# Kernel tuning notes

Hardware: AMD Instinct MI355X
Metric: run time of the kernel (lower is better)

Reference implementation:

```python
import jax, jax.numpy as jnp
import numpy as np

# Static config (matches init_kwargs)
B, L, D = 4, 4096, 1024
K, H, M = 32, 32, 1           # key heads, per-head dim, num_thetas
A = 4                          # num_anchor_heads
CK = 4                         # conv_kernel_size (causal depthwise)
D_INNER = D                    # expand_factor = 1
ZC = 2 * D_INNER + K           # in_proj output channels = 2080
FLAT = K * H * M
SPLIT = H * M


def setup_inputs() -> dict:
    key = jax.random.key(0)
    ks = jax.random.split(key, 6)
    x = jax.random.normal(ks[0], (B, L, D), jnp.float32)
    # in_proj Dense(d_inner*2 + K, no bias): [D, ZC]
    W_in = jax.random.normal(ks[1], (D, ZC), jnp.float32) / np.sqrt(D)
    # depthwise causal conv kernel, flax 'WIO' layout: [CK, 1, ZC]
    conv_kernel = jax.random.normal(ks[2], (CK, 1, ZC), jnp.float32) / np.sqrt(CK)
    # theta init for M == 1: linspace grid with alternating signs
    grid = np.linspace(0.1, 1.5, K * H).reshape(1, 1, K, H, 1)
    signs = np.resize([1.0, -1.0], grid.shape)
    theta = jnp.asarray(grid * signs, jnp.float32)
    # inverse-softplus of geomspace slopes
    decay_slopes = jnp.asarray(np.log(np.exp(np.geomspace(0.001, 0.1, K - A)) - 1.0), jnp.float32)
    anchor_slopes = jnp.asarray(np.log(np.exp(np.geomspace(0.01, 0.1, A)) - 1.0), jnp.float32)
    score_scale = jnp.ones((K,), jnp.float32)
    lim = float(np.sqrt(6.0 / (SPLIT + H)))  # glorot uniform
    W_re = jax.random.uniform(ks[3], (SPLIT, H), jnp.float32, -lim, lim)
    W_im = jax.random.uniform(ks[4], (SPLIT, H), jnp.float32, -lim, lim)
    norm_scale = jnp.ones((2 * SPLIT,), jnp.float32)
    W_out = jax.random.normal(ks[5], (D_INNER, D), jnp.float32) / np.sqrt(D_INNER)
    return {"x": x, "W_in": W_in, "conv_kernel": conv_kernel, "theta": theta,
            "decay_slopes": decay_slopes, "anchor_slopes": anchor_slopes,
            "score_scale": score_scale, "W_re": W_re, "W_im": W_im,
            "norm_scale": norm_scale, "W_out": W_out}


def reference(x, W_in, conv_kernel, theta, decay_slopes, anchor_slopes,
              score_scale, W_re, W_im, norm_scale, W_out):
    b, l, _ = x.shape
    z = x @ W_in                                           # [b,l,ZC]
    # causal depthwise conv (padding (CK-1, 0), groups == channels)
    z = jax.lax.conv_general_dilated(
        z, conv_kernel, window_strides=(1,), padding=((CK - 1, 0),),
        dimension_numbers=('NWC', 'WIO', 'NWC'), feature_group_count=ZC)
    x_val = z[..., :D_INNER].reshape(b, l, K, H)
    x_gate = jax.nn.silu(z[..., D_INNER:2 * D_INNER])      # [b,l,d_inner]
    s_raw = z[..., -K:].reshape(b, l, K, 1)
    # ALiBi-style log time weights: decay heads look back, anchor heads decay from start
    pos = jnp.arange(l, dtype=jnp.float32)
    dist = jnp.maximum(jnp.float32(l - 1) - pos, 0.0)      # maxlen=None -> l
    log_w = jnp.concatenate([
        -jax.nn.softplus(decay_slopes).reshape(1, 1, -1, 1) * dist[None, :, None, None],
        -jax.nn.softplus(anchor_slopes).reshape(1, 1, -1, 1) * pos[None, :, None, None],
    ], axis=2)                                             # [1,l,K,1]
    p_w = jnp.exp(score_scale[None, None, :, None] * s_raw + log_w)  # [b,l,K,1]
    # complex phase features
    phi = x_val[..., None] * theta                         # [b,l,K,H,M]
    pwb = p_w[..., None]
    num_re_in = (pwb * jnp.cos(phi)).reshape(b, l, FLAT)
    num_im_in = (pwb * jnp.sin(phi)).reshape(b, l, FLAT)
    merged = jnp.concatenate([p_w.squeeze(-1), num_re_in, num_im_in], axis=-1)
    cs = jnp.cumsum(merged, axis=1)                        # causal prefix sum over seq
    den, num_re, num_im = jnp.split(cs, [K, K + FLAT], axis=-1)
    inv_den = 1.0 / jnp.maximum(den.reshape(b, l, K, 1), 1e-4)
    re = num_re.reshape(b, l, K, SPLIT) * inv_den
    im = num_im.reshape(b, l, K, SPLIT) * inv_den
    # running RMS normalization over complex features
    mean_sq = (jnp.sum(re * re, -1) + jnp.sum(im * im, -1)) / (2 * SPLIT)
    rs = jax.lax.rsqrt(mean_sq[..., None] + 1e-5)
    y = (re * rs * norm_scale[:SPLIT]) @ W_re + (im * rs * norm_scale[SPLIT:]) @ W_im  # [b,l,K,H]
    return (y.reshape(b, l, D_INNER) * x_gate) @ W_out
```

## Files before the change

kernel.cpp:

```cpp
#include <hip/hip_runtime.h>
#include <hip/hip_bf16.h>
#include <math.h>

#define BB 4
#define LL 4096
#define DD 1024
#define KK 32
#define HH 32
#define AA 4
#define CKK 4
#define DI 1024
#define ZC 2080
#define FLATC 1024
#define BL (BB * LL)
#define ZLD 2080
#define NPAD 2176

#define CCH 32
#define NCHK (LL / CCH)

#define GLD 1136
#define KLD 1080

typedef unsigned short u16;
typedef __attribute__((ext_vector_type(8))) short s16x8;
typedef __attribute__((ext_vector_type(4))) float f32x4;

__device__ __forceinline__ u16 f2bf(float f) {
  union { float f; unsigned int u; } v; v.f = f;
  unsigned int r = (v.u + 0x7FFFu + ((v.u >> 16) & 1u)) >> 16;
  return (u16)r;
}
__device__ __forceinline__ float bf2f(u16 u) {
  union { unsigned int i; float f; } x; x.i = ((unsigned int)u) << 16; return x.f;
}
__device__ __forceinline__ void gl_lds16(const void* g, void* l) {
  __builtin_amdgcn_global_load_lds(
      (const __attribute__((address_space(1))) unsigned int*)g,
      (__attribute__((address_space(3))) unsigned int*)l, 16, 0, 0);
}

__global__ __launch_bounds__(256) void cast_bf16_kernel(
    const float* __restrict__ src, u16* __restrict__ dst, int n) {
  const int i = (blockIdx.x * 256 + threadIdx.x) * 8;
  if (i >= n) return;
  float4 a = *(const float4*)(src + i);
  float4 b = *(const float4*)(src + i + 4);
  s16x8 v;
  v[0] = (short)f2bf(a.x); v[1] = (short)f2bf(a.y);
  v[2] = (short)f2bf(a.z); v[3] = (short)f2bf(a.w);
  v[4] = (short)f2bf(b.x); v[5] = (short)f2bf(b.y);
  v[6] = (short)f2bf(b.z); v[7] = (short)f2bf(b.w);
  *(s16x8*)(dst + i) = v;
}

__global__ __launch_bounds__(256) void transpose_cast_kernel(
    const float* __restrict__ src, u16* __restrict__ dst,
    int R, int C, int Cpad) {
  __shared__ float t[32][33];
  const int tid = threadIdx.x;
  const int r0 = blockIdx.x * 32, c0 = blockIdx.y * 32;
  const int lr = tid >> 5, lc = tid & 31;
#pragma unroll
  for (int i = 0; i < 4; ++i) {
    const int r = r0 + i * 8 + lr, c = c0 + lc;
    float v = 0.f;
    if (r < R && c < C) v = src[(size_t)r * C + c];
    t[lc][i * 8 + lr] = v;
  }
  __syncthreads();
#pragma unroll
  for (int i = 0; i < 4; ++i) {
    const int dr = c0 + i * 8 + lr;
    const int dc = r0 + lc;
    if (dr < Cpad && dc < R) dst[(size_t)dr * R + dc] = f2bf(t[i * 8 + lr][lc]);
  }
}

#define FENCE() asm volatile("" ::: "memory")
#define SBAR() do { FENCE(); __builtin_amdgcn_s_barrier(); FENCE(); } while (0)
#define VMCNT6() asm volatile("s_waitcnt vmcnt(6)" ::: "memory")

#define RA(s, h) (((s) * 2 + (h)) * 8192)
#define RB(s, h) (32768 + ((s) * 2 + (h)) * 8192)

template <int OUT_BF16>
__global__ __launch_bounds__(512, 2) void gemm256_8ph(
    const u16* __restrict__ A, const u16* __restrict__ Bt, void* __restrict__ C,
    int lda, int ldb, int ldc, int Kd, int Ncols) {
  __shared__ u16 lds[65536];
  const int tid = threadIdx.x;
  const int lane = tid & 63, wv = tid >> 6;
  const int wm = wv >> 2, wn = wv & 3;
  const int lm = lane & 15, lq = lane >> 4;
  const int bm = blockIdx.x * 256, bn = blockIdx.y * 256;
  const int NT = Kd >> 6;
  const int NT2 = NT >> 1;

  const int rofs = wv * 8 + (lane >> 3);
  const int cel = ((lane & 7) ^ (lane >> 3)) * 8;

  auto stageH = [&](const u16* __restrict__ G, int rowBase, int ld, int kt,
                    int regU16) {
    const u16* g0 = G + (size_t)(rowBase + rofs) * ld + (kt << 6) + cel;
    gl_lds16(g0, &lds[regU16 + wv * 512]);
    const u16* g1 = G + (size_t)(rowBase + 64 + rofs) * ld + (kt << 6) + cel;
    gl_lds16(g1, &lds[regU16 + 4096 + wv * 512]);
  };

  s16x8 Af[4][2], Bf[4][2];
  f32x4 acc[8][4];
  const f32x4 z4 = {0.f, 0.f, 0.f, 0.f};
#pragma unroll
  for (int i = 0; i < 8; ++i)
#pragma unroll
    for (int j = 0; j < 4; ++j) acc[i][j] = z4;

  const int xorw = (lm & 7) << 3;

#define DSA(s, mh)                                                          \
  _Pragma("unroll") for (int f = 0; f < 4; ++f)                             \
  _Pragma("unroll") for (int ks = 0; ks < 2; ++ks)                          \
    Af[f][ks] = *(const s16x8*)&lds[RA(s, wm) +                             \
      (((((mh) * 4 + f) * 16 + lm) * 64 + ((ks * 32 + lq * 8) ^ xorw)))];

#define DSB(s)                                                              \
  _Pragma("unroll") for (int f = 0; f < 4; ++f)                             \
  _Pragma("unroll") for (int ks = 0; ks < 2; ++ks)                          \
    Bf[f][ks] = *(const s16x8*)&lds[RB(s, wn >> 1) +                        \
      ((((wn & 1) * 64 + f * 16 + lm) * 64 + ((ks * 32 + lq * 8) ^ xorw)))];

#define QUAD(mh, nh)                                                        \
  do {                                                                      \
    __builtin_amdgcn_s_setprio(1);                                          \
    _Pragma("unroll") for (int f = 0; f < 4; ++f)                           \
    _Pragma("unroll") for (int n = 0; n < 2; ++n)                           \
    _Pragma("unroll") for (int ks = 0; ks < 2; ++ks)                        \
      acc[(mh) * 4 + f][(nh) * 2 + n] =                                     \
          __builtin_amdgcn_mfma_f32_16x16x32_bf16(                          \
              Af[f][ks], Bf[(nh) * 2 + n][ks],                              \
              acc[(mh) * 4 + f][(nh) * 2 + n], 0, 0, 0);                    \
    __builtin_amdgcn_s_setprio(0);                                          \
  } while (0)

  stageH(A, bm, lda, 0, RA(0, 0));
  stageH(A, bm + 128, lda, 0, RA(0, 1));
  stageH(Bt, bn, ldb, 0, RB(0, 0));
  stageH(Bt, bn + 128, ldb, 0, RB(0, 1));
  stageH(Bt, bn, ldb, 1, RB(1, 0));
  stageH(Bt, bn + 128, ldb, 1, RB(1, 1));
  stageH(A, bm, lda, 1, RA(1, 0));
  VMCNT6();
  SBAR();

#pragma unroll 1
  for (int t = 0; t < NT2; ++t) {
    const int T2 = 2 * t + 2, T3 = 2 * t + 3;
    DSA(0, 0); DSB(0);
    stageH(A, bm + 128, lda, 2 * t + 1, RA(1, 1));
    SBAR();
    QUAD(0, 0);
    SBAR();
    if (T2 < NT) stageH(Bt, bn, ldb, T2, RB(0, 0));
    SBAR();
    QUAD(0, 1);
    SBAR();
    DSA(0, 1);
    if (T2 < NT) stageH(Bt, bn + 128, ldb, T2, RB(0, 1));
    SBAR();
    QUAD(1, 0);
    SBAR();
    if (T2 < NT) stageH(A, bm, lda, T2, RA(0, 0));
    SBAR();
    QUAD(1, 1);
    VMCNT6();
    SBAR();
    DSA(1, 0); DSB(1);
    if (T2 < NT) stageH(A, bm + 128, lda, T2, RA(0, 1));
    SBAR();
    QUAD(0, 0);
    SBAR();
    if (T3 < NT) stageH(Bt, bn, ldb, T3, RB(1, 0));
    SBAR();
    QUAD(0, 1);
    SBAR();
    DSA(1, 1);
    if (T3 < NT) stageH(Bt, bn + 128, ldb, T3, RB(1, 1));
    SBAR();
    QUAD(1, 0);
    SBAR();
    if (T3 < NT) stageH(A, bm, lda, T3, RA(1, 0));
    SBAR();
    QUAD(1, 1);
    VMCNT6();
    SBAR();
  }

#pragma unroll
  for (int f = 0; f < 8; ++f) {
#pragma unroll
    for (int n = 0; n < 4; ++n) {
#pragma unroll
      for (int r = 0; r < 4; ++r) {
        const int row = bm + wm * 128 + f * 16 + lq * 4 + r;
        const int col = bn + wn * 64 + n * 16 + lm;
        if (col < Ncols) {
          if (OUT_BF16)
            ((u16*)C)[(size_t)row * ldc + col] = f2bf(acc[f][n][r]);
          else
            ((float*)C)[(size_t)row * ldc + col] = acc[f][n][r];
        }
      }
    }
  }
#undef DSA
#undef DSB
#undef QUAD
}

__global__ __launch_bounds__(256) void score_gemm(
    const u16* __restrict__ A, const u16* __restrict__ Bt,
    u16* __restrict__ z) {
  __shared__ u16 As[8192];
  __shared__ u16 Bs[2048];
  const int tid = threadIdx.x;
  const int lane = tid & 63, wv = tid >> 6;
  const int lm = lane & 15, lq = lane >> 4;
  const int bm = blockIdx.x * 128;

  const f32x4 z4 = {0.f, 0.f, 0.f, 0.f};
  f32x4 acc[2][2];
#pragma unroll
  for (int i = 0; i < 2; ++i)
#pragma unroll
    for (int j = 0; j < 2; ++j) acc[i][j] = z4;

  for (int k0 = 0; k0 < DD; k0 += 64) {
    __syncthreads();
#pragma unroll
    for (int t = 0; t < 5; ++t) {
      const int idx = wv * 5 + t;
      if (idx < 16) {
        const int mt = idx >> 1, kt = idx & 1;
        const u16* g = A + (size_t)(bm + mt * 16 + lm) * DD + k0 + kt * 32 + lq * 8;
        gl_lds16(g, &As[idx * 512]);
      } else {
        const int bidx = idx - 16;
        const int nt = bidx >> 1, kt = bidx & 1;
        const u16* g = Bt + (size_t)(2048 + nt * 16 + lm) * DD + k0 + kt * 32 + lq * 8;
        gl_lds16(g, &Bs[bidx * 512]);
      }
    }
    __syncthreads();
#pragma unroll
    for (int kt = 0; kt < 2; ++kt) {
      s16x8 af[2], bfb[2];
#pragma unroll
      for (int i = 0; i < 2; ++i) {
        const int mt = wv * 2 + i;
        af[i] = *(const s16x8*)&As[(mt * 2 + kt) * 512 + lane * 8];
        bfb[i] = *(const s16x8*)&Bs[(i * 2 + kt) * 512 + lane * 8];
      }
#pragma unroll
      for (int i = 0; i < 2; ++i)
#pragma unroll
        for (int j = 0; j < 2; ++j)
          acc[i][j] = __builtin_amdgcn_mfma_f32_16x16x32_bf16(af[i], bfb[j], acc[i][j], 0, 0, 0);
    }
  }
#pragma unroll
  for (int i = 0; i < 2; ++i)
#pragma unroll
    for (int j = 0; j < 2; ++j)
#pragma unroll
      for (int r = 0; r < 4; ++r) {
        const int row = bm + wv * 32 + i * 16 + lq * 4 + r;
        const int col = 2048 + j * 16 + lm;
        z[(size_t)row * ZLD + col] = f2bf(acc[i][j][r]);
      }
}

__global__ __launch_bounds__(256) void conv_feat_scan(
    const u16* __restrict__ z, const float* __restrict__ kern,
    const float* __restrict__ theta, const float* __restrict__ decay,
    const float* __restrict__ anchor, const float* __restrict__ sscale,
    float* __restrict__ merged, float* __restrict__ part) {
  __shared__ float pbuf[CCH][KK];
  const int tid = threadIdx.x;
  const int r0 = blockIdx.x * CCH;
  const bool first = ((r0 & (LL - 1)) == 0);
  const int chunk = blockIdx.x;

#pragma unroll
  for (int q = 0; q < 4; ++q) {
    const int item = q * 256 + tid;
    const int row = item >> 5, k = item & 31;
    float v = 0.f;
#pragma unroll
    for (int w = 0; w < CKK; ++w) {
      const int g = row + w;
      float zv = 0.f;
      if (!(first && g < 3))
        zv = bf2f(z[(size_t)(r0 - 3 + g) * ZLD + 2048 + k]);
      v = fmaf(zv, kern[w * ZC + 2048 + k], v);
    }
    const int l = (r0 + row) & (LL - 1);
    const float slope = (k < KK - AA) ? decay[k] : anchor[k - (KK - AA)];
    const float sp = log1pf(__expf(slope));
    const float lw = (k < KK - AA) ? (-sp * (float)(LL - 1 - l)) : (-sp * (float)l);
    pbuf[row][k] = __expf(sscale[k] * v + lw);
  }
  __syncthreads();

  if (tid < KK) {
    float run = 0.f;
#pragma unroll
    for (int row = 0; row < CCH; ++row) {
      run += pbuf[row][tid];
      merged[(size_t)(r0 + row) * ZC + tid] = run;
    }
    part[(size_t)chunk * ZC + tid] = run;
  }

#pragma unroll 1
  for (int it = 0; it < 4; ++it) {
    const int c = it * 256 + tid;
    const float kw0 = kern[0 * ZC + c], kw1 = kern[1 * ZC + c];
    const float kw2 = kern[2 * ZC + c], kw3 = kern[3 * ZC + c];
    const float th = theta[c];
    const int head = c >> 5;
    float h0 = 0.f, h1 = 0.f, h2 = 0.f;
    if (!first) {
      h0 = bf2f(z[(size_t)(r0 - 3) * ZLD + c]);
      h1 = bf2f(z[(size_t)(r0 - 2) * ZLD + c]);
      h2 = bf2f(z[(size_t)(r0 - 1) * ZLD + c]);
    }
    float sre = 0.f, sim = 0.f;
#pragma unroll 4
    for (int row = 0; row < CCH; ++row) {
      const float h3 = bf2f(z[(size_t)(r0 + row) * ZLD + c]);
      float v = h0 * kw0;
      v = fmaf(h1, kw1, v);
      v = fmaf(h2, kw2, v);
      v = fmaf(h3, kw3, v);
      h0 = h1; h1 = h2; h2 = h3;
      const float phi = v * th;
      float sv, cv;
      __sincosf(phi, &sv, &cv);
      const float p = pbuf[row][head];
      sre = fmaf(p, cv, sre);
      sim = fmaf(p, sv, sim);
      float* mrow = merged + (size_t)(r0 + row) * ZC;
      mrow[KK + c] = sre;
      mrow[KK + FLATC + c] = sim;
    }
    part[(size_t)chunk * ZC + KK + c] = sre;
    part[(size_t)chunk * ZC + KK + FLATC + c] = sim;
  }
}

__global__ __launch_bounds__(256) void scan_offsets_kernel(float* __restrict__ part) {
  const int c = blockIdx.x * 256 + threadIdx.x;
  const int b = blockIdx.z;
  if (c >= ZC) return;
  float run = 0.f;
#pragma unroll 8
  for (int i = 0; i < NCHK; ++i) {
    const size_t idx = ((size_t)b * NCHK + i) * ZC + c;
    const float t = part[idx];
    part[idx] = run;
    run += t;
  }
}

__global__ __launch_bounds__(256) void wprime_kernel(
    const float* __restrict__ W_re, const float* __restrict__ W_im,
    const float* __restrict__ ns, u16* __restrict__ wp) {
  const int i = blockIdx.x * 256 + threadIdx.x;
  if (i < 1024) wp[i] = f2bf(ns[i >> 5] * W_re[i]);
  else {
    const int j = i - 1024;
    wp[i] = f2bf(ns[32 + (j >> 5)] * W_im[j]);
  }
}

__global__ __launch_bounds__(256) void norm_head_mfma(
    float* merged, const u16* __restrict__ z, const float* __restrict__ kern,
    const u16* __restrict__ wp, const float* __restrict__ part) {
  __shared__ u16 zw[11 * GLD];
  __shared__ float skern[4 * KLD];
  const int tid = threadIdx.x;
  const int r0 = blockIdx.x * 8;
  const bool first = ((r0 & (LL - 1)) == 0);
  const int lane = tid & 63, wv = tid >> 6;
  const int lm = lane & 15, lq = lane >> 4;
  const float* po = part + (size_t)(blockIdx.x >> 2) * ZC;

  for (int idx = tid; idx < 11 * 128; idx += 256) {
    const int i = idx >> 7, c8 = idx & 127;
    s16x8 v = {0, 0, 0, 0, 0, 0, 0, 0};
    if (!(first && i < 3))
      v = *(const s16x8*)(z + (size_t)(r0 - 3 + i) * ZLD + 1024 + c8 * 8);
    *(s16x8*)&zw[i * GLD + c8 * 8 + (c8 >> 4) * 16] = v;
  }
  for (int idx = tid; idx < 4 * 256; idx += 256) {
    const int w = idx >> 8, c4 = idx & 255;
    float4 v = *(const float4*)(kern + w * ZC + 1024 + c4 * 4);
    *(float4*)&skern[w * KLD + c4 * 4 + (c4 >> 5) * 8] = v;
  }

  s16x8 bre[2], bim[2];
#pragma unroll
  for (int nt = 0; nt < 2; ++nt)
#pragma unroll
    for (int jj = 0; jj < 8; ++jj) {
      bre[nt][jj] = (short)wp[(lq * 8 + jj) * 32 + nt * 16 + lm];
      bim[nt][jj] = (short)wp[1024 + (lq * 8 + jj) * 32 + nt * 16 + lm];
    }
  __syncthreads();

  const f32x4 z4 = {0.f, 0.f, 0.f, 0.f};
#pragma unroll 1
  for (int rr2 = 0; rr2 < 2; ++rr2) {
    const int rr = wv * 2 + rr2;
    const int bl = r0 + rr;
    float* row = merged + (size_t)bl * ZC;
    const float den0 = row[lm] + po[lm];
    const float den1 = row[16 + lm] + po[16 + lm];

#pragma unroll
    for (int khalf = 0; khalf < 2; ++khalf) {
      const int co = KK + (khalf * 16 + lm) * 32 + lq * 8;
      const float* rp = row + co;
      const float* pp = po + co;
      float4 ra = *(const float4*)rp;
      float4 rb = *(const float4*)(rp + 4);
      float4 ia = *(const float4*)(rp + FLATC);
      float4 ib = *(const float4*)(rp + FLATC + 4);
      float4 qa = *(const float4*)pp;
      float4 qb = *(const float4*)(pp + 4);
      float4 ja = *(const float4*)(pp + FLATC);
      float4 jb = *(const float4*)(pp + FLATC + 4);
      ra.x += qa.x; ra.y += qa.y; ra.z += qa.z; ra.w += qa.w;
      rb.x += qb.x; rb.y += qb.y; rb.z += qb.z; rb.w += qb.w;
      ia.x += ja.x; ia.y += ja.y; ia.z += ja.z; ia.w += ja.w;
      ib.x += jb.x; ib.y += jb.y; ib.z += jb.z; ib.w += jb.w;

      float ssq = ra.x * ra.x + ra.y * ra.y + ra.z * ra.z + ra.w * ra.w +
                  rb.x * rb.x + rb.y * rb.y + rb.z * rb.z + rb.w * rb.w +
                  ia.x * ia.x + ia.y * ia.y + ia.z * ia.z + ia.w * ia.w +
                  ib.x * ib.x + ib.y * ib.y + ib.z * ib.z + ib.w * ib.w;
      ssq += __shfl_xor(ssq, 16);
      ssq += __shfl_xor(ssq, 32);
      const float den = khalf ? den1 : den0;
      const float inv = 1.0f / fmaxf(den, 1e-4f);
      const float scale = inv * rsqrtf(ssq * inv * inv * (1.0f / 64.0f) + 1e-5f);

      s16x8 afr, afi;
      afr[0] = (short)f2bf(ra.x * scale); afr[1] = (short)f2bf(ra.y * scale);
      afr[2] = (short)f2bf(ra.z * scale); afr[3] = (short)f2bf(ra.w * scale);
      afr[4] = (short)f2bf(rb.x * scale); afr[5] = (short)f2bf(rb.y * scale);
      afr[6] = (short)f2bf(rb.z * scale); afr[7] = (short)f2bf(rb.w * scale);
      afi[0] = (short)f2bf(ia.x * scale); afi[1] = (short)f2bf(ia.y * scale);
      afi[2] = (short)f2bf(ia.z * scale); afi[3] = (short)f2bf(ia.w * scale);
      afi[4] = (short)f2bf(ib.x * scale); afi[5] = (short)f2bf(ib.y * scale);
      afi[6] = (short)f2bf(ib.z * scale); afi[7] = (short)f2bf(ib.w * scale);

      f32x4 acc[2];
#pragma unroll
      for (int nt = 0; nt < 2; ++nt) {
        acc[nt] = __builtin_amdgcn_mfma_f32_16x16x32_bf16(afr, bre[nt], z4, 0, 0, 0);
        acc[nt] = __builtin_amdgcn_mfma_f32_16x16x32_bf16(afi, bim[nt], acc[nt], 0, 0, 0);
      }

      u16* grow = (u16*)row;
#pragma unroll
      for (int nt = 0; nt < 2; ++nt) {
#pragma unroll
        for (int r = 0; r < 4; ++r) {
          const int k = khalf * 16 + lq * 4 + r;
          const int o = k * 32 + nt * 16 + lm;
          const int sk = o + (o >> 7) * 8;
          const int sz = o + (o >> 7) * 16;
          float gv = bf2f(zw[(rr + 0) * GLD + sz]) * skern[0 * KLD + sk];
          gv = fmaf(bf2f(zw[(rr + 1) * GLD + sz]), skern[1 * KLD + sk], gv);
          gv = fmaf(bf2f(zw[(rr + 2) * GLD + sz]), skern[2 * KLD + sk], gv);
          gv = fmaf(bf2f(zw[(rr + 3) * GLD + sz]), skern[3 * KLD + sk], gv);
          const float sil = gv * (1.0f / (1.0f + __expf(-gv)));
          grow[o] = f2bf(acc[nt][r] * sil);
        }
      }
    }
  }
}

extern "C" void kernel_launch(void* const* d_in, const int* in_sizes, int n_in,
                              void* d_out, int out_size, void* d_ws, size_t ws_size,
                              hipStream_t stream) {
  const float* x      = (const float*)d_in[0];
  const float* W_in   = (const float*)d_in[1];
  const float* kern   = (const float*)d_in[2];
  const float* theta  = (const float*)d_in[3];
  const float* decay  = (const float*)d_in[4];
  const float* anchor = (const float*)d_in[5];
  const float* sscale = (const float*)d_in[6];
  const float* W_re   = (const float*)d_in[7];
  const float* W_im   = (const float*)d_in[8];
  const float* nscale = (const float*)d_in[9];
  const float* W_out  = (const float*)d_in[10];
  float* out = (float*)d_out;

  char* w = (char*)d_ws;
  float* merged = (float*)w;
  u16* xbf = (u16*)w;
  u16* zbf = (u16*)(w + (size_t)BL * ZC * 4);
  u16* wobt = zbf;
  u16* wp = (u16*)(w + (size_t)BL * ZC * 4 + (size_t)BL * ZLD * 2);
  u16* wbt = wp + 2048;
  float* part = (float*)wbt;

  cast_bf16_kernel<<<dim3(BL * DD / 8 / 256), 256, 0, stream>>>(x, xbf, BL * DD);
  transpose_cast_kernel<<<dim3(32, 68), 256, 0, stream>>>(W_in, wbt, DD, ZC, NPAD);
  wprime_kernel<<<dim3(8), 256, 0, stream>>>(W_re, W_im, nscale, wp);

  score_gemm<<<dim3(BL / 128), 256, 0, stream>>>(xbf, wbt, zbf);

  gemm256_8ph<1><<<dim3(BL / 256, 8), 512, 0, stream>>>(
      xbf, wbt, zbf, DD, DD, ZLD, DD, ZC);

  conv_feat_scan<<<dim3(BL / CCH), 256, 0, stream>>>(
      zbf, kern, theta, decay, anchor, sscale, merged, part);

  {
    dim3 grid2((ZC + 255) / 256, 1, BB);
    scan_offsets_kernel<<<grid2, 256, 0, stream>>>(part);
  }

  norm_head_mfma<<<dim3(BL / 8), 256, 0, stream>>>(merged, zbf, kern, wp, part);

  transpose_cast_kernel<<<dim3(32, 32), 256, 0, stream>>>(W_out, wobt, DI, DD, DD);
  gemm256_8ph<0><<<dim3(BL / 256, DD / 256), 512, 0, stream>>>(
      (const u16*)merged, wobt, out, 2 * ZC, DI, DD, DI, DD);
}
```

Before: 364.2 us.

## Fuse conv, features, scan and norm-head per head with two-pass segmented scan

Replaces the materialized fp32 prefix-sum buffer (merged), the chunk-offset scan and the separate norm/head kernel with a head-major two-pass design. The in_proj GEMM and score GEMM now write z in a [b,k,l,h] layout. A first pass computes per-segment totals of the weighted cos/sin features and densities. A small scan turns those totals into segment offsets. A second pass recomputes the conv and phase features, scans them in shared memory, normalizes, applies W_re/W_im in registers, gates with the SiLU conv output, and writes bf16 directly. This removes the large fp32 intermediate write/read traffic. The cost is computing the sincos features twice, only 512 blocks each walking 1024 rows sequentially, and scattered stores in the GEMM epilogue.

```diff
diff --git a/kernel.cpp b/kernel.cpp
--- a/kernel.cpp
+++ b/kernel.cpp
@@ -13,14 +13,9 @@
 #define ZC 2080
 #define FLATC 1024
 #define BL (BB * LL)
-#define ZLD 2080
 #define NPAD 2176
-
-#define CCH 32
-#define NCHK (LL / CCH)
-
-#define GLD 1136
-#define KLD 1080
+#define SEG 4
+#define FST 68
 
 typedef unsigned short u16;
 typedef __attribute__((ext_vector_type(8))) short s16x8;
@@ -84,10 +79,10 @@
 #define RA(s, h) (((s) * 2 + (h)) * 8192)
 #define RB(s, h) (32768 + ((s) * 2 + (h)) * 8192)
 
-template <int OUT_BF16>
+template <int MODE>
 __global__ __launch_bounds__(512, 2) void gemm256_8ph(
     const u16* __restrict__ A, const u16* __restrict__ Bt, void* __restrict__ C,
-    int lda, int ldb, int ldc, int Kd, int Ncols) {
+    void* __restrict__ C2, int lda, int ldb, int ldc, int Kd, int Ncols) {
   __shared__ u16 lds[65536];
   const int tid = threadIdx.x;
   const int lane = tid & 63, wv = tid >> 6;
@@ -200,15 +195,19 @@
   for (int f = 0; f < 8; ++f) {
 #pragma unroll
     for (int n = 0; n < 4; ++n) {
+      const int c = bn + wn * 64 + n * 16 + lm;
 #pragma unroll
       for (int r = 0; r < 4; ++r) {
         const int row = bm + wm * 128 + f * 16 + lq * 4 + r;
-        const int col = bn + wn * 64 + n * 16 + lm;
-        if (col < Ncols) {
-          if (OUT_BF16)
-            ((u16*)C)[(size_t)row * ldc + col] = f2bf(acc[f][n][r]);
-          else
-            ((float*)C)[(size_t)row * ldc + col] = acc[f][n][r];
+        if (MODE == 0) {
+          if (c < Ncols)
+            ((float*)C)[(size_t)row * ldc + c] = acc[f][n][r];
+        } else {
+          const int b2 = row >> 12, l2 = row & 4095;
+          const int k2 = (c >> 5) & 31, h2 = c & 31;
+          u16* dst = (c < 1024) ? (u16*)C : (u16*)C2;
+          dst[((size_t)(b2 * 32 + k2) * 4096 + l2) * 32 + h2] =
+              f2bf(acc[f][n][r]);
         }
       }
     }
@@ -220,7 +219,7 @@
 
 __global__ __launch_bounds__(256) void score_gemm(
     const u16* __restrict__ A, const u16* __restrict__ Bt,
-    u16* __restrict__ z) {
+    u16* __restrict__ z2s) {
   __shared__ u16 As[8192];
   __shared__ u16 Bs[2048];
   const int tid = threadIdx.x;
@@ -275,222 +274,254 @@
 #pragma unroll
       for (int r = 0; r < 4; ++r) {
         const int row = bm + wv * 32 + i * 16 + lq * 4 + r;
-        const int col = 2048 + j * 16 + lm;
-        z[(size_t)row * ZLD + col] = f2bf(acc[i][j][r]);
-      }
-}
-
-__global__ __launch_bounds__(256) void conv_feat_scan(
-    const u16* __restrict__ z, const float* __restrict__ kern,
+        const int b2 = row >> 12, l2 = row & 4095;
+        const int k2 = j * 16 + lm;
+        z2s[(size_t)(b2 * 32 + k2) * 4096 + l2] = f2bf(acc[i][j][r]);
+      }
+}
+
+__global__ __launch_bounds__(256) void fuse_pass0(
+    const u16* __restrict__ z2x, const u16* __restrict__ z2s,
+    const float* __restrict__ kern, const float* __restrict__ theta,
+    const float* __restrict__ decay, const float* __restrict__ anchor,
+    const float* __restrict__ sscale, float* __restrict__ tot) {
+  __shared__ u16 zx[67 * 32];
+  __shared__ float zs[68];
+  __shared__ float pw[64];
+  __shared__ float kx[4][32], th[32];
+  __shared__ float ks4[4];
+  __shared__ float red[8][64];
+  __shared__ float dred[64];
+
+  const int tid = threadIdx.x;
+  const int bk = blockIdx.x;
+  const int s = blockIdx.y;
+  const int k = bk & 31;
+  const int rr = tid >> 5, h = tid & 31;
+  const size_t pbase = (size_t)bk * 4096 * 32;
+  const size_t sbase = (size_t)bk * 4096;
+
+  if (tid < 128) {
+    const int w_ = tid >> 5, c = tid & 31;
+    kx[w_][c] = kern[w_ * ZC + k * 32 + c];
+  }
+  if (tid < 32) th[tid] = theta[k * 32 + tid];
+  if (tid < 4) ks4[tid] = kern[tid * ZC + 2048 + k];
+  const float slope = (k < KK - AA) ? decay[k] : anchor[k - (KK - AA)];
+  const float sp = log1pf(__expf(slope));
+  const float sk = sscale[k];
+  __syncthreads();
+
+  const int l0 = s * 1024;
+  float sre_acc = 0.f, sim_acc = 0.f, den_acc = 0.f;
+
+#pragma unroll 1
+  for (int ch = 0; ch < 16; ++ch) {
+    const int r0 = l0 + ch * 64;
+    for (int u = tid; u < 268; u += 256) {
+      const int row = u >> 2, q = u & 3;
+      const int gl = r0 - 3 + row;
+      s16x8 vx = {0, 0, 0, 0, 0, 0, 0, 0};
+      if (gl >= 0) vx = *(const s16x8*)(z2x + pbase + (size_t)gl * 32 + q * 8);
+      *(s16x8*)&zx[row * 32 + q * 8] = vx;
+    }
+    if (tid < 67) {
+      const int gl = r0 - 3 + tid;
+      zs[tid] = (gl >= 0) ? bf2f(z2s[sbase + gl]) : 0.f;
+    }
+    __syncthreads();
+    if (tid < 64) {
+      float v = zs[tid] * ks4[0];
+      v = fmaf(zs[tid + 1], ks4[1], v);
+      v = fmaf(zs[tid + 2], ks4[2], v);
+      v = fmaf(zs[tid + 3], ks4[3], v);
+      const int l = r0 + tid;
+      const float lw = (k < KK - AA) ? (-sp * (float)(LL - 1 - l))
+                                     : (-sp * (float)l);
+      const float p = __expf(sk * v + lw);
+      pw[tid] = p;
+      den_acc += p;
+    }
+    __syncthreads();
+#pragma unroll
+    for (int rg = 0; rg < 8; ++rg) {
+      const int r = rg * 8 + rr;
+      float v = bf2f(zx[r * 32 + h]) * kx[0][h];
+      v = fmaf(bf2f(zx[(r + 1) * 32 + h]), kx[1][h], v);
+      v = fmaf(bf2f(zx[(r + 2) * 32 + h]), kx[2][h], v);
+      v = fmaf(bf2f(zx[(r + 3) * 32 + h]), kx[3][h], v);
+      float sv, cv;
+      __sincosf(v * th[h], &sv, &cv);
+      const float p = pw[r];
+      sre_acc = fmaf(p, cv, sre_acc);
+      sim_acc = fmaf(p, sv, sim_acc);
+    }
+    __syncthreads();
+  }
+
+  red[rr][h] = sre_acc;
+  red[rr][h + 32] = sim_acc;
+  if (tid < 64) dred[tid] = den_acc;
+  __syncthreads();
+  const int fl = bk * SEG + s;
+  if (tid < 64) {
+    float t0 = 0.f;
+#pragma unroll
+    for (int i = 0; i < 8; ++i) t0 += red[i][tid];
+    tot[(size_t)fl * 72 + tid] = t0;
+  } else if (tid == 64) {
+    float t0 = 0.f;
+#pragma unroll
+    for (int i = 0; i < 64; ++i) t0 += dred[i];
+    tot[(size_t)fl * 72 + 64] = t0;
+  }
+}
+
+__global__ __launch_bounds__(128) void seg_scan(float* __restrict__ tot) {
+  const int bk = blockIdx.x, tid = threadIdx.x;
+  if (tid >= 65) return;
+  float run = 0.f;
+#pragma unroll
+  for (int s = 0; s < SEG; ++s) {
+    const size_t idx = (size_t)(bk * SEG + s) * 72 + tid;
+    const float t = tot[idx];
+    tot[idx] = run;
+    run += t;
+  }
+}
+
+__global__ __launch_bounds__(256) void fuse_pass1(
+    const u16* __restrict__ z2x, const u16* __restrict__ z2g,
+    const u16* __restrict__ z2s, const float* __restrict__ kern,
     const float* __restrict__ theta, const float* __restrict__ decay,
     const float* __restrict__ anchor, const float* __restrict__ sscale,
-    float* __restrict__ merged, float* __restrict__ part) {
-  __shared__ float pbuf[CCH][KK];
+    const float* __restrict__ W_re, const float* __restrict__ W_im,
+    const float* __restrict__ ns, const float* __restrict__ tot,
+    u16* __restrict__ g) {
+  __shared__ u16 zx[67 * 32];
+  __shared__ u16 zg[67 * 32];
+  __shared__ float zs[68];
+  __shared__ float f[64 * FST];
+  __shared__ float pw[64];
+  __shared__ float kx[4][32], kg[4][32], th[32];
+  __shared__ float ks4[4];
+
   const int tid = threadIdx.x;
-  const int r0 = blockIdx.x * CCH;
-  const bool first = ((r0 & (LL - 1)) == 0);
-  const int chunk = blockIdx.x;
-
-#pragma unroll
-  for (int q = 0; q < 4; ++q) {
-    const int item = q * 256 + tid;
-    const int row = item >> 5, k = item & 31;
-    float v = 0.f;
-#pragma unroll
-    for (int w = 0; w < CKK; ++w) {
-      const int g = row + w;
-      float zv = 0.f;
-      if (!(first && g < 3))
-        zv = bf2f(z[(size_t)(r0 - 3 + g) * ZLD + 2048 + k]);
-      v = fmaf(zv, kern[w * ZC + 2048 + k], v);
-    }
-    const int l = (r0 + row) & (LL - 1);
-    const float slope = (k < KK - AA) ? decay[k] : anchor[k - (KK - AA)];
-    const float sp = log1pf(__expf(slope));
-    const float lw = (k < KK - AA) ? (-sp * (float)(LL - 1 - l)) : (-sp * (float)l);
-    pbuf[row][k] = __expf(sscale[k] * v + lw);
+  const int bk = blockIdx.x;
+  const int s = blockIdx.y;
+  const int k = bk & 31;
+  const int b = bk >> 5;
+  const int rr = tid >> 5, h = tid & 31;
+  const size_t pbase = (size_t)bk * 4096 * 32;
+  const size_t sbase = (size_t)bk * 4096;
+
+  if (tid < 128) {
+    const int w_ = tid >> 5, c = tid & 31;
+    kx[w_][c] = kern[w_ * ZC + k * 32 + c];
+    kg[w_][c] = kern[w_ * ZC + 1024 + k * 32 + c];
+  }
+  if (tid < 32) th[tid] = theta[k * 32 + tid];
+  if (tid < 4) ks4[tid] = kern[tid * ZC + 2048 + k];
+  const float slope = (k < KK - AA) ? decay[k] : anchor[k - (KK - AA)];
+  const float sp = log1pf(__expf(slope));
+  const float sk = sscale[k];
+  float wre[32], wim[32];
+#pragma unroll
+  for (int hp = 0; hp < 32; ++hp) {
+    wre[hp] = ns[hp] * W_re[hp * 32 + h];
+    wim[hp] = ns[32 + hp] * W_im[hp * 32 + h];
   }
   __syncthreads();
 
-  if (tid < KK) {
-    float run = 0.f;
-#pragma unroll
-    for (int row = 0; row < CCH; ++row) {
-      run += pbuf[row][tid];
-      merged[(size_t)(r0 + row) * ZC + tid] = run;
-    }
-    part[(size_t)chunk * ZC + tid] = run;
-  }
+  const int l0 = s * 1024;
+  const int fl = bk * SEG + s;
+  float run = (tid < 65) ? tot[(size_t)fl * 72 + tid] : 0.f;
 
 #pragma unroll 1
-  for (int it = 0; it < 4; ++it) {
-    const int c = it * 256 + tid;
-    const float kw0 = kern[0 * ZC + c], kw1 = kern[1 * ZC + c];
-    const float kw2 = kern[2 * ZC + c], kw3 = kern[3 * ZC + c];
-    const float th = theta[c];
-    const int head = c >> 5;
-    float h0 = 0.f, h1 = 0.f, h2 = 0.f;
-    if (!first) {
-      h0 = bf2f(z[(size_t)(r0 - 3) * ZLD + c]);
-      h1 = bf2f(z[(size_t)(r0 - 2) * ZLD + c]);
-      h2 = bf2f(z[(size_t)(r0 - 1) * ZLD + c]);
-    }
-    float sre = 0.f, sim = 0.f;
-#pragma unroll 4
-    for (int row = 0; row < CCH; ++row) {
-      const float h3 = bf2f(z[(size_t)(r0 + row) * ZLD + c]);
-      float v = h0 * kw0;
-      v = fmaf(h1, kw1, v);
-      v = fmaf(h2, kw2, v);
-      v = fmaf(h3, kw3, v);
-      h0 = h1; h1 = h2; h2 = h3;
-      const float phi = v * th;
+  for (int ch = 0; ch < 16; ++ch) {
+    const int r0 = l0 + ch * 64;
+    for (int u = tid; u < 268; u += 256) {
+      const int row = u >> 2, q = u & 3;
+      const int gl = r0 - 3 + row;
+      s16x8 vx = {0, 0, 0, 0, 0, 0, 0, 0}, vg = vx;
+      if (gl >= 0) {
+        vx = *(const s16x8*)(z2x + pbase + (size_t)gl * 32 + q * 8);
+        vg = *(const s16x8*)(z2g + pbase + (size_t)gl * 32 + q * 8);
+      }
+      *(s16x8*)&zx[row * 32 + q * 8] = vx;
+      *(s16x8*)&zg[row * 32 + q * 8] = vg;
+    }
+    if (tid < 67) {
+      const int gl = r0 - 3 + tid;
+      zs[tid] = (gl >= 0) ? bf2f(z2s[sbase + gl]) : 0.f;
+    }
+    __syncthreads();
+    if (tid < 64) {
+      float v = zs[tid] * ks4[0];
+      v = fmaf(zs[tid + 1], ks4[1], v);
+      v = fmaf(zs[tid + 2], ks4[2], v);
+      v = fmaf(zs[tid + 3], ks4[3], v);
+      const int l = r0 + tid;
+      const float lw = (k < KK - AA) ? (-sp * (float)(LL - 1 - l))
+                                     : (-sp * (float)l);
+      pw[tid] = __expf(sk * v + lw);
+    }
+    __syncthreads();
+#pragma unroll
+    for (int rg = 0; rg < 8; ++rg) {
+      const int r = rg * 8 + rr;
+      float v = bf2f(zx[r * 32 + h]) * kx[0][h];
+      v = fmaf(bf2f(zx[(r + 1) * 32 + h]), kx[1][h], v);
+      v = fmaf(bf2f(zx[(r + 2) * 32 + h]), kx[2][h], v);
+      v = fmaf(bf2f(zx[(r + 3) * 32 + h]), kx[3][h], v);
       float sv, cv;
-      __sincosf(phi, &sv, &cv);
-      const float p = pbuf[row][head];
-      sre = fmaf(p, cv, sre);
-      sim = fmaf(p, sv, sim);
-      float* mrow = merged + (size_t)(r0 + row) * ZC;
-      mrow[KK + c] = sre;
-      mrow[KK + FLATC + c] = sim;
-    }
-    part[(size_t)chunk * ZC + KK + c] = sre;
-    part[(size_t)chunk * ZC + KK + FLATC + c] = sim;
-  }
-}
-
-__global__ __launch_bounds__(256) void scan_offsets_kernel(float* __restrict__ part) {
-  const int c = blockIdx.x * 256 + threadIdx.x;
-  const int b = blockIdx.z;
-  if (c >= ZC) return;
-  float run = 0.f;
-#pragma unroll 8
-  for (int i = 0; i < NCHK; ++i) {
-    const size_t idx = ((size_t)b * NCHK + i) * ZC + c;
-    const float t = part[idx];
-    part[idx] = run;
-    run += t;
-  }
-}
-
-__global__ __launch_bounds__(256) void wprime_kernel(
-    const float* __restrict__ W_re, const float* __restrict__ W_im,
-    const float* __restrict__ ns, u16* __restrict__ wp) {
-  const int i = blockIdx.x * 256 + threadIdx.x;
-  if (i < 1024) wp[i] = f2bf(ns[i >> 5] * W_re[i]);
-  else {
-    const int j = i - 1024;
-    wp[i] = f2bf(ns[32 + (j >> 5)] * W_im[j]);
-  }
-}
-
-__global__ __launch_bounds__(256) void norm_head_mfma(
-    float* merged, const u16* __restrict__ z, const float* __restrict__ kern,
-    const u16* __restrict__ wp, const float* __restrict__ part) {
-  __shared__ u16 zw[11 * GLD];
-  __shared__ float skern[4 * KLD];
-  const int tid = threadIdx.x;
-  const int r0 = blockIdx.x * 8;
-  const bool first = ((r0 & (LL - 1)) == 0);
-  const int lane = tid & 63, wv = tid >> 6;
-  const int lm = lane & 15, lq = lane >> 4;
-  const float* po = part + (size_t)(blockIdx.x >> 2) * ZC;
-
-  for (int idx = tid; idx < 11 * 128; idx += 256) {
-    const int i = idx >> 7, c8 = idx & 127;
-    s16x8 v = {0, 0, 0, 0, 0, 0, 0, 0};
-    if (!(first && i < 3))
-      v = *(const s16x8*)(z + (size_t)(r0 - 3 + i) * ZLD + 1024 + c8 * 8);
-    *(s16x8*)&zw[i * GLD + c8 * 8 + (c8 >> 4) * 16] = v;
-  }
-  for (int idx = tid; idx < 4 * 256; idx += 256) {
-    const int w = idx >> 8, c4 = idx & 255;
-    float4 v = *(const float4*)(kern + w * ZC + 1024 + c4 * 4);
-    *(float4*)&skern[w * KLD + c4 * 4 + (c4 >> 5) * 8] = v;
-  }
-
-  s16x8 bre[2], bim[2];
-#pragma unroll
-  for (int nt = 0; nt < 2; ++nt)
-#pragma unroll
-    for (int jj = 0; jj < 8; ++jj) {
-      bre[nt][jj] = (short)wp[(lq * 8 + jj) * 32 + nt * 16 + lm];
-      bim[nt][jj] = (short)wp[1024 + (lq * 8 + jj) * 32 + nt * 16 + lm];
-    }
-  __syncthreads();
-
-  const f32x4 z4 = {0.f, 0.f, 0.f, 0.f};
-#pragma unroll 1
-  for (int rr2 = 0; rr2 < 2; ++rr2) {
-    const int rr = wv * 2 + rr2;
-    const int bl = r0 + rr;
-    float* row = merged + (size_t)bl * ZC;
-    const float den0 = row[lm] + po[lm];
-    const float den1 = row[16 + lm] + po[16 + lm];
-
-#pragma unroll
-    for (int khalf = 0; khalf < 2; ++khalf) {
-      const int co = KK + (khalf * 16 + lm) * 32 + lq * 8;
-      const float* rp = row + co;
-      const float* pp = po + co;
-      float4 ra = *(const float4*)rp;
-      float4 rb = *(const float4*)(rp + 4);
-      float4 ia = *(const float4*)(rp + FLATC);
-      float4 ib = *(const float4*)(rp + FLATC + 4);
-      float4 qa = *(const float4*)pp;
-      float4 qb = *(const float4*)(pp + 4);
-      float4 ja = *(const float4*)(pp + FLATC);
-      float4 jb = *(const float4*)(pp + FLATC + 4);
-      ra.x += qa.x; ra.y += qa.y; ra.z += qa.z; ra.w += qa.w;
-      rb.x += qb.x; rb.y += qb.y; rb.z += qb.z; rb.w += qb.w;
-      ia.x += ja.x; ia.y += ja.y; ia.z += ja.z; ia.w += ja.w;
-      ib.x += jb.x; ib.y += jb.y; ib.z += jb.z; ib.w += jb.w;
-
-      float ssq = ra.x * ra.x + ra.y * ra.y + ra.z * ra.z + ra.w * ra.w +
-                  rb.x * rb.x + rb.y * rb.y + rb.z * rb.z + rb.w * rb.w +
-                  ia.x * ia.x + ia.y * ia.y + ia.z * ia.z + ia.w * ia.w +
-                  ib.x * ib.x + ib.y * ib.y + ib.z * ib.z + ib.w * ib.w;
-      ssq += __shfl_xor(ssq, 16);
-      ssq += __shfl_xor(ssq, 32);
-      const float den = khalf ? den1 : den0;
+      __sincosf(v * th[h], &sv, &cv);
+      const float p = pw[r];
+      f[r * FST + h] = p * cv;
+      f[r * FST + 32 + h] = p * sv;
+      if (h == 0) f[r * FST + 64] = p;
+    }
+    __syncthreads();
+    if (tid < 65) {
+      float rn = run;
+#pragma unroll
+      for (int r = 0; r < 64; ++r) {
+        rn += f[r * FST + tid];
+        f[r * FST + tid] = rn;
+      }
+      run = rn;
+    }
+    __syncthreads();
+#pragma unroll
+    for (int rg = 0; rg < 8; ++rg) {
+      const int r = rg * 8 + rr;
+      const float xre = f[r * FST + h], xim = f[r * FST + 32 + h];
+      float part = fmaf(xre, xre, xim * xim);
+      part += __shfl_xor(part, 1);
+      part += __shfl_xor(part, 2);
+      part += __shfl_xor(part, 4);
+      part += __shfl_xor(part, 8);
+      part += __shfl_xor(part, 16);
+      const float den = f[r * FST + 64];
       const float inv = 1.0f / fmaxf(den, 1e-4f);
-      const float scale = inv * rsqrtf(ssq * inv * inv * (1.0f / 64.0f) + 1e-5f);
-
-      s16x8 afr, afi;
-      afr[0] = (short)f2bf(ra.x * scale); afr[1] = (short)f2bf(ra.y * scale);
-      afr[2] = (short)f2bf(ra.z * scale); afr[3] = (short)f2bf(ra.w * scale);
-      afr[4] = (short)f2bf(rb.x * scale); afr[5] = (short)f2bf(rb.y * scale);
-      afr[6] = (short)f2bf(rb.z * scale); afr[7] = (short)f2bf(rb.w * scale);
-      afi[0] = (short)f2bf(ia.x * scale); afi[1] = (short)f2bf(ia.y * scale);
-      afi[2] = (short)f2bf(ia.z * scale); afi[3] = (short)f2bf(ia.w * scale);
-      afi[4] = (short)f2bf(ib.x * scale); afi[5] = (short)f2bf(ib.y * scale);
-      afi[6] = (short)f2bf(ib.z * scale); afi[7] = (short)f2bf(ib.w * scale);
-
-      f32x4 acc[2];
-#pragma unroll
-      for (int nt = 0; nt < 2; ++nt) {
-        acc[nt] = __builtin_amdgcn_mfma_f32_16x16x32_bf16(afr, bre[nt], z4, 0, 0, 0);
-        acc[nt] = __builtin_amdgcn_mfma_f32_16x16x32_bf16(afi, bim[nt], acc[nt], 0, 0, 0);
-      }
-
-      u16* grow = (u16*)row;
-#pragma unroll
-      for (int nt = 0; nt < 2; ++nt) {
-#pragma unroll
-        for (int r = 0; r < 4; ++r) {
-          const int k = khalf * 16 + lq * 4 + r;
-          const int o = k * 32 + nt * 16 + lm;
-          const int sk = o + (o >> 7) * 8;
-          const int sz = o + (o >> 7) * 16;
-          float gv = bf2f(zw[(rr + 0) * GLD + sz]) * skern[0 * KLD + sk];
-          gv = fmaf(bf2f(zw[(rr + 1) * GLD + sz]), skern[1 * KLD + sk], gv);
-          gv = fmaf(bf2f(zw[(rr + 2) * GLD + sz]), skern[2 * KLD + sk], gv);
-          gv = fmaf(bf2f(zw[(rr + 3) * GLD + sz]), skern[3 * KLD + sk], gv);
-          const float sil = gv * (1.0f / (1.0f + __expf(-gv)));
-          grow[o] = f2bf(acc[nt][r] * sil);
-        }
-      }
-    }
+      const float scale =
+          inv * rsqrtf(part * inv * inv * (1.0f / 64.0f) + 1e-5f);
+      float y = 0.f;
+#pragma unroll
+      for (int hp = 0; hp < 32; ++hp) {
+        y = fmaf(f[r * FST + hp], wre[hp], y);
+        y = fmaf(f[r * FST + 32 + hp], wim[hp], y);
+      }
+      y *= scale;
+      float gv = bf2f(zg[r * 32 + h]) * kg[0][h];
+      gv = fmaf(bf2f(zg[(r + 1) * 32 + h]), kg[1][h], gv);
+      gv = fmaf(bf2f(zg[(r + 2) * 32 + h]), kg[2][h], gv);
+      gv = fmaf(bf2f(zg[(r + 3) * 32 + h]), kg[3][h], gv);
+      const float sil = gv * (1.0f / (1.0f + __expf(-gv)));
+      const int l = r0 + r;
+      g[((size_t)(b * 4096 + l)) * 1024 + k * 32 + h] = f2bf(y * sil);
+    }
+    __syncthreads();
   }
 }
 
@@ -511,34 +542,31 @@
   float* out = (float*)d_out;
 
   char* w = (char*)d_ws;
-  float* merged = (float*)w;
-  u16* xbf = (u16*)w;
-  u16* zbf = (u16*)(w + (size_t)BL * ZC * 4);
-  u16* wobt = zbf;
-  u16* wp = (u16*)(w + (size_t)BL * ZC * 4 + (size_t)BL * ZLD * 2);
-  u16* wbt = wp + 2048;
-  float* part = (float*)wbt;
+  u16* xbf   = (u16*)w;
+  u16* z2x   = (u16*)(w + 33554432ull);
+  u16* z2g   = (u16*)(w + 67108864ull);
+  u16* z2s   = (u16*)(w + 100663296ull);
+  u16* g     = (u16*)(w + 101711872ull);
+  u16* wbt   = (u16*)(w + 135266304ull);
+  float* tot = (float*)(w + 139722752ull);
+  u16* wobt  = z2x;
 
   cast_bf16_kernel<<<dim3(BL * DD / 8 / 256), 256, 0, stream>>>(x, xbf, BL * DD);
   transpose_cast_kernel<<<dim3(32, 68), 256, 0, stream>>>(W_in, wbt, DD, ZC, NPAD);
-  wprime_kernel<<<dim3(8), 256, 0, stream>>>(W_re, W_im, nscale, wp);
-
-  score_gemm<<<dim3(BL / 128), 256, 0, stream>>>(xbf, wbt, zbf);
-
-  gemm256_8ph<1><<<dim3(BL / 256, 8), 512, 0, stream>>>(
-      xbf, wbt, zbf, DD, DD, ZLD, DD, ZC);
-
-  conv_feat_scan<<<dim3(BL / CCH), 256, 0, stream>>>(
-      zbf, kern, theta, decay, anchor, sscale, merged, part);
-
-  {
-    dim3 grid2((ZC + 255) / 256, 1, BB);
-    scan_offsets_kernel<<<grid2, 256, 0, stream>>>(part);
-  }
-
-  norm_head_mfma<<<dim3(BL / 8), 256, 0, stream>>>(merged, zbf, kern, wp, part);
+
+  score_gemm<<<dim3(BL / 128), 256, 0, stream>>>(xbf, wbt, z2s);
+
+  gemm256_8ph<2><<<dim3(BL / 256, 8), 512, 0, stream>>>(
+      xbf, wbt, z2x, z2g, DD, DD, 0, DD, 2048);
+
+  fuse_pass0<<<dim3(BB * KK, SEG), 256, 0, stream>>>(
+      z2x, z2s, kern, theta, decay, anchor, sscale, tot);
+  seg_scan<<<dim3(BB * KK), 128, 0, stream>>>(tot);
+  fuse_pass1<<<dim3(BB * KK, SEG), 256, 0, stream>>>(
+      z2x, z2g, z2s, kern, theta, decay, anchor, sscale,
+      W_re, W_im, nscale, tot, g);
 
   transpose_cast_kernel<<<dim3(32, 32), 256, 0, stream>>>(W_out, wobt, DI, DD, DD);
   gemm256_8ph<0><<<dim3(BL / 256, DD / 256), 512, 0, stream>>>(
-      (const u16*)merged, wobt, out, 2 * ZC, DI, DD, DI, DD);
-}
+      g, wobt, out, nullptr, DI, DD, DD, DI, DD);
+}
```

Measured after the change: 413.2 us. 1.13x slower.
